# Kernel tuning notes

Measured on AMD Instinct MI355X. Metric: run time of the kernel, lower is better.

Reference implementation:

```python
import jax, jax.numpy as jnp
import numpy as np
import functools

N_NODES = 16
WIDTH = 64
C_DIM = 3
LATENT_DIM = 8
B = 131072


def build_graph(n=N_NODES, k=4, p=0.75, seed=0):
    """Watts-Strogatz-style random graph oriented low->high node id (DAG),
    mirroring build_random_graph(nodes, 1 input, 1 output, p=0.75, k=4)."""
    rng = np.random.RandomState(seed)
    edges = set()
    for i in range(n):
        for d in range(1, k // 2 + 1):
            j = (i + d) % n
            if rng.rand() < p:
                j = int(rng.randint(n))
            a, b = min(i, j), max(i, j)
            if a != b:
                edges.add((a, b))
    preds = [set() for _ in range(n)]
    for a, b in edges:
        preds[b].add(a)
    # every non-source node must have a predecessor (connectivity)
    for j in range(1, n):
        if not preds[j]:
            a = int(rng.randint(j))
            preds[j].add(a)
            edges.add((a, j))
    succs = [set() for _ in range(n)]
    for a, b in edges:
        succs[a].add(b)
    preds = [sorted(p_) for p_ in preds]
    sources = [j for j in range(n) if not preds[j]]   # receive the INR feature f
    sinks = [j for j in range(n) if not succs[j]]     # combined into the single output
    return preds, sources, sinks


def gaussian(x):
    return jnp.exp(-0.5 * x * x)

# 'large' activation set for graph nodes, assigned deterministically per node
GRAPH_ACTS = [jnp.tanh, jax.nn.elu, jax.nn.softplus, jnp.sin, gaussian]


def setup_inputs() -> dict:
    key = jax.random.key(0)
    ks = jax.random.split(key, 16)

    def nrm(k, shape, s):
        return jax.random.normal(k, shape, dtype=jnp.float32) * s

    inputs = jax.random.normal(ks[0], (B, 3, 1), dtype=jnp.float32)   # (x, y, r) coords
    latents = jax.random.normal(ks[1], (B, LATENT_DIM), dtype=jnp.float32)
    Wl = nrm(ks[2], (WIDTH, LATENT_DIM), 0.3)
    bl = jnp.zeros((WIDTH,), jnp.float32)
    Wx = nrm(ks[3], (WIDTH, 1), 1.0)
    Wy = nrm(ks[4], (WIDTH, 1), 1.0)
    Wr = nrm(ks[5], (WIDTH, 1), 1.0)
    W1 = nrm(ks[6], (WIDTH, WIDTH), 0.15)
    b1 = jnp.zeros((WIDTH,), jnp.float32)
    gW = nrm(ks[7], (N_NODES, WIDTH, WIDTH), 0.15)   # per-graph-node Linear(width,width)
    gB = jnp.zeros((N_NODES, WIDTH), jnp.float32)
    outW = nrm(ks[8], (C_DIM, WIDTH), 0.15)          # combine -> c_dim output
    outb = jnp.zeros((C_DIM,), jnp.float32)
    scale = jnp.ones((1,), jnp.float32)              # ScaleAct learnable scalar
    return {"inputs": inputs, "latents": latents, "Wl": Wl, "bl": bl, "Wx": Wx,
            "Wy": Wy, "Wr": Wr, "W1": W1, "b1": b1, "gW": gW, "gB": gB,
            "outW": outW, "outb": outb, "scale": scale}


def reference(inputs, latents, Wl, bl, Wx, Wy, Wr, W1, b1, gW, gB, outW, outb, scale):
    x, y, r = inputs[:, 0, :], inputs[:, 1, :], inputs[:, 2, :]   # each (B, 1)
    latents_ = jnp.tanh(latents @ Wl.T + bl)      # acts_start[0] = Tanh
    r_ = jax.nn.elu(r @ Wr.T)                     # acts_start[1] = ELU
    y_ = jax.nn.softplus(y @ Wy.T)                # acts_start[2] = Softplus
    x_ = jnp.tanh(x @ Wx.T)                       # acts_start[3] = Tanh
    f = gaussian(x_ + y_ + r_ + latents_)         # acts_start[4] = Gaussian
    f = jnp.sin(f @ W1.T + b1)                    # acts_start[5] = SinLayer

    # random-topology graph network: gather(sum preds) -> linear -> activation
    preds, sources, sinks = build_graph()
    hs = []
    for j in range(N_NODES):
        if j in sources:
            inp = f
        else:
            inp = functools.reduce(lambda a, b_: a + b_, [hs[i] for i in preds[j]])
        hs.append(GRAPH_ACTS[j % len(GRAPH_ACTS)](inp @ gW[j].T + gB[j]))
    agg = functools.reduce(lambda a, b_: a + b_, [hs[j] for j in sinks])
    res = (agg @ outW.T + outb) * scale           # combine + ScaleAct
    return jax.nn.sigmoid(res)                    # final_activation='sigmoid'
```

## Files before the change

kernel.cpp:

```cpp
#include <hip/hip_runtime.h>
#include <cstdint>

#define NN 16
#define W64 64
#define MT 64
#define NSTAGE 17

typedef _Float16 half8   __attribute__((ext_vector_type(8)));
typedef _Float16 half16  __attribute__((ext_vector_type(16)));
typedef float    floatx4 __attribute__((ext_vector_type(4)));

struct GraphCfg {
    unsigned pred[NN];
    unsigned sinkmask;
};

__device__ __forceinline__ float act_tanh(float x)     { return 1.0f - 2.0f / (1.0f + __expf(2.0f * x)); }
__device__ __forceinline__ float act_elu(float x)      { return x > 0.0f ? x : __expf(x) - 1.0f; }
__device__ __forceinline__ float act_softplus(float x) { return fmaxf(x, 0.0f) + __logf(1.0f + __expf(-fabsf(x))); }
__device__ __forceinline__ float act_gauss(float x)    { return __expf(-0.5f * x * x); }

__device__ __forceinline__ float apply_act(int a, float x) {
    switch (a) {
        case 0:  return act_tanh(x);
        case 1:  return act_elu(x);
        case 2:  return act_softplus(x);
        case 3:  return __sinf(x);
        default: return act_gauss(x);
    }
}

__device__ __forceinline__ half8 cvt8(float4 a, float4 b) {
    half8 h;
    h[0]=(_Float16)a.x; h[1]=(_Float16)a.y; h[2]=(_Float16)a.z; h[3]=(_Float16)a.w;
    h[4]=(_Float16)b.x; h[5]=(_Float16)b.y; h[6]=(_Float16)b.z; h[7]=(_Float16)b.w;
    return h;
}

__global__ __launch_bounds__(256, 2) void inr_mfma_kernel(
    const float* __restrict__ inputs, const float* __restrict__ latents,
    const float* __restrict__ Wl, const float* __restrict__ bl,
    const float* __restrict__ Wx, const float* __restrict__ Wy,
    const float* __restrict__ Wr, const float* __restrict__ W1,
    const float* __restrict__ b1, const float* __restrict__ gW,
    const float* __restrict__ gB, const float* __restrict__ outW,
    const float* __restrict__ outb, const float* __restrict__ scale,
    float* __restrict__ out, int Btot, GraphCfg cfg)
{
    __shared__ __align__(16) _Float16 inpbuf[2][MT * W64];
    __shared__ __align__(16) _Float16 wbuf[2][W64 * W64];

    const int tid  = threadIdx.x;
    const int lane = tid & 63;
    const int wv   = tid >> 6;
    const int q    = lane >> 4;
    const int c    = lane & 15;
    const int rowbase = wv * 16;
    const int m0   = blockIdx.x * MT;

    half16 hreg[NSTAGE];

    {
        const int em = tid >> 2, ep = tid & 3;
        int mg = m0 + em; if (mg >= Btot) mg = Btot - 1;
        const float x = inputs[mg * 3 + 0];
        const float y = inputs[mg * 3 + 1];
        const float r = inputs[mg * 3 + 2];
        const float4 l0 = *(const float4*)(latents + mg * 8);
        const float4 l1 = *(const float4*)(latents + mg * 8 + 4);
        #pragma unroll
        for (int i = 0; i < 16; ++i) {
            const int k = ep * 16 + i;
            const float4 a = *(const float4*)(Wl + k * 8);
            const float4 b = *(const float4*)(Wl + k * 8 + 4);
            float ld = bl[k];
            ld = fmaf(l0.x, a.x, ld); ld = fmaf(l0.y, a.y, ld);
            ld = fmaf(l0.z, a.z, ld); ld = fmaf(l0.w, a.w, ld);
            ld = fmaf(l1.x, b.x, ld); ld = fmaf(l1.y, b.y, ld);
            ld = fmaf(l1.z, b.z, ld); ld = fmaf(l1.w, b.w, ld);
            const float tk = act_tanh(x * Wx[k]) + act_softplus(y * Wy[k])
                           + act_elu(r * Wr[k]) + act_tanh(ld);
            inpbuf[0][em * W64 + k] = (_Float16)act_gauss(tk);
        }
    }
    {
        const float4* src = (const float4*)W1;
        const float4 f0 = src[2 * tid],       f1 = src[2 * tid + 1];
        const float4 f2 = src[2 * tid + 512], f3 = src[2 * tid + 513];
        ((half8*)wbuf[0])[tid]       = cvt8(f0, f1);
        ((half8*)wbuf[0])[tid + 256] = cvt8(f2, f3);
    }
    __syncthreads();

    #pragma unroll
    for (int s = 0; s < NSTAGE; ++s) {
        const int slot = s & 1;

        float4 nf0, nf1, nf2, nf3;
        if (s + 1 < NSTAGE) {
            const float4* src = (const float4*)(gW + s * 4096);
            nf0 = src[2 * tid];       nf1 = src[2 * tid + 1];
            nf2 = src[2 * tid + 512]; nf3 = src[2 * tid + 513];
        }

        const half8 a0 = *(const half8*)&inpbuf[slot][(rowbase + c) * W64 +  0 + q * 8];
        const half8 a1 = *(const half8*)&inpbuf[slot][(rowbase + c) * W64 + 32 + q * 8];

        floatx4 acc[4];
        #pragma unroll
        for (int t = 0; t < 4; ++t) {
            const half8 b0  = *(const half8*)&wbuf[slot][(t * 16 + c) * W64 +  0 + q * 8];
            const half8 b1f = *(const half8*)&wbuf[slot][(t * 16 + c) * W64 + 32 + q * 8];
            floatx4 z = {0.f, 0.f, 0.f, 0.f};
            z = __builtin_amdgcn_mfma_f32_16x16x32_f16(a0, b0, z, 0, 0, 0);
            z = __builtin_amdgcn_mfma_f32_16x16x32_f16(a1, b1f, z, 0, 0, 0);
            acc[t] = z;
        }

        const float* bias = (s == 0) ? b1 : (gB + (s - 1) * W64);
        const int an   = (s == 0) ? 3 : ((s - 1) % 5);
        const int hidx = (s == 0) ? 16 : (s - 1);
        #pragma unroll
        for (int t = 0; t < 4; ++t) {
            const float bs = bias[t * 16 + c];
            #pragma unroll
            for (int r = 0; r < 4; ++r) {
                const float v = apply_act(an, acc[t][r] + bs);
                hreg[hidx][t * 4 + r] = (_Float16)v;
            }
        }

        if (s + 1 < NSTAGE) {
            const int node = s;
            const unsigned pm = cfg.pred[node];
            float sf[16];
            if (pm == 0u) {
                #pragma unroll
                for (int v = 0; v < 16; ++v) sf[v] = (float)hreg[16][v];
            } else {
                #pragma unroll
                for (int v = 0; v < 16; ++v) sf[v] = 0.0f;
                #pragma unroll
                for (int i = 0; i < NN; ++i) {
                    if (pm & (1u << i)) {
                        #pragma unroll
                        for (int v = 0; v < 16; ++v) sf[v] += (float)hreg[i][v];
                    }
                }
            }
            const int wslot = (s + 1) & 1;
            #pragma unroll
            for (int t = 0; t < 4; ++t)
                #pragma unroll
                for (int r = 0; r < 4; ++r)
                    inpbuf[wslot][(rowbase + q * 4 + r) * W64 + t * 16 + c] =
                        (_Float16)sf[t * 4 + r];
            ((half8*)wbuf[wslot])[tid]       = cvt8(nf0, nf1);
            ((half8*)wbuf[wslot])[tid + 256] = cvt8(nf2, nf3);
        }
        __syncthreads();
    }

    {
        float sf[16];
        #pragma unroll
        for (int v = 0; v < 16; ++v) sf[v] = 0.0f;
        #pragma unroll
        for (int j = 0; j < NN; ++j) {
            if (cfg.sinkmask & (1u << j)) {
                #pragma unroll
                for (int v = 0; v < 16; ++v) sf[v] += (float)hreg[j][v];
            }
        }
        #pragma unroll
        for (int t = 0; t < 4; ++t)
            #pragma unroll
            for (int r = 0; r < 4; ++r)
                inpbuf[1][(rowbase + q * 4 + r) * W64 + t * 16 + c] =
                    (_Float16)sf[t * 4 + r];
    }
    __syncthreads();
    {
        const int em = tid >> 2, ep = tid & 3;
        float p0 = 0.f, p1 = 0.f, p2 = 0.f;
        #pragma unroll
        for (int h = 0; h < 2; ++h) {
            const half8 hv = *(const half8*)&inpbuf[1][em * W64 + ep * 16 + h * 8];
            #pragma unroll
            for (int i = 0; i < 8; ++i) {
                const float av = (float)hv[i];
                const int k = ep * 16 + h * 8 + i;
                p0 = fmaf(av, outW[0 * W64 + k], p0);
                p1 = fmaf(av, outW[1 * W64 + k], p1);
                p2 = fmaf(av, outW[2 * W64 + k], p2);
            }
        }
        p0 += __shfl_xor(p0, 1); p0 += __shfl_xor(p0, 2);
        p1 += __shfl_xor(p1, 1); p1 += __shfl_xor(p1, 2);
        p2 += __shfl_xor(p2, 1); p2 += __shfl_xor(p2, 2);
        const int mg = m0 + em;
        if (ep < 3 && mg < Btot) {
            const float pr = (ep == 0) ? p0 : ((ep == 1) ? p1 : p2);
            const float res = (pr + outb[ep]) * scale[0];
            out[mg * 3 + ep] = 1.0f / (1.0f + __expf(-res));
        }
    }
}

namespace {

struct NpMT {
    unsigned mt[624];
    int mti;
    explicit NpMT(unsigned s) {
        mt[0] = s;
        for (int i = 1; i < 624; ++i)
            mt[i] = 1812433253u * (mt[i-1] ^ (mt[i-1] >> 30)) + (unsigned)i;
        mti = 624;
    }
    unsigned next() {
        if (mti >= 624) {
            for (int i = 0; i < 624; ++i) {
                const unsigned y = (mt[i] & 0x80000000u) | (mt[(i+1) % 624] & 0x7fffffffu);
                unsigned v = mt[(i+397) % 624] ^ (y >> 1);
                if (y & 1u) v ^= 0x9908b0dfu;
                mt[i] = v;
            }
            mti = 0;
        }
        unsigned y = mt[mti++];
        y ^= y >> 11;
        y ^= (y << 7)  & 0x9d2c5680u;
        y ^= (y << 15) & 0xefc60000u;
        y ^= y >> 18;
        return y;
    }
    double rnd() {
        const unsigned a = next() >> 5;
        const unsigned b = next() >> 6;
        return (a * 67108864.0 + b) / 9007199254740992.0;
    }
    long randint(long n) {
        const unsigned long maxv = (unsigned long)n - 1;
        if (maxv == 0) return 0;
        unsigned long mask = maxv;
        mask |= mask >> 1;  mask |= mask >> 2;  mask |= mask >> 4;
        mask |= mask >> 8;  mask |= mask >> 16;
        unsigned long v;
        do { v = (unsigned long)next() & mask; } while (v > maxv);
        return (long)v;
    }
};

static GraphCfg build_graph_cfg() {
    NpMT rng(0u);
    bool edge[NN][NN] = {};
    for (int i = 0; i < NN; ++i) {
        for (int d = 1; d <= 2; ++d) {
            int j = (i + d) & (NN - 1);
            if (rng.rnd() < 0.75) j = (int)rng.randint(NN);
            const int a = i < j ? i : j;
            const int b = i < j ? j : i;
            if (a != b) edge[a][b] = true;
        }
    }
    GraphCfg cfg{};
    for (int a = 0; a < NN; ++a)
        for (int b = 0; b < NN; ++b)
            if (edge[a][b]) cfg.pred[b] |= 1u << a;
    for (int j = 1; j < NN; ++j) {
        if (!cfg.pred[j]) {
            const int a = (int)rng.randint(j);
            cfg.pred[j] |= 1u << a;
            edge[a][j] = true;
        }
    }
    unsigned succ[NN] = {};
    for (int a = 0; a < NN; ++a)
        for (int b = 0; b < NN; ++b)
            if (edge[a][b]) succ[a] |= 1u << b;
    cfg.sinkmask = 0u;
    for (int j = 0; j < NN; ++j)
        if (!succ[j]) cfg.sinkmask |= 1u << j;
    return cfg;
}

}

extern "C" void kernel_launch(void* const* d_in, const int* in_sizes, int n_in,
                              void* d_out, int out_size, void* d_ws, size_t ws_size,
                              hipStream_t stream)
{
    const float* inputs  = (const float*)d_in[0];
    const float* latents = (const float*)d_in[1];
    const float* Wl      = (const float*)d_in[2];
    const float* bl      = (const float*)d_in[3];
    const float* Wx      = (const float*)d_in[4];
    const float* Wy      = (const float*)d_in[5];
    const float* Wr      = (const float*)d_in[6];
    const float* W1      = (const float*)d_in[7];
    const float* b1      = (const float*)d_in[8];
    const float* gW      = (const float*)d_in[9];
    const float* gB      = (const float*)d_in[10];
    const float* outW    = (const float*)d_in[11];
    const float* outb    = (const float*)d_in[12];
    const float* scale   = (const float*)d_in[13];
    float* out = (float*)d_out;

    const int Btot = in_sizes[0] / 3;
    const GraphCfg cfg = build_graph_cfg();

    const int blocks = (Btot + MT - 1) / MT;
    inr_mfma_kernel<<<blocks, 256, 0, stream>>>(
        inputs, latents, Wl, bl, Wx, Wy, Wr, W1, b1, gW, gB, outW, outb, scale,
        out, Btot, cfg);
}
```

Before: 223.3 us.

## Pad LDS rows, sum predecessors in fp16, raise occupancy target

Pads the shared-memory activation and weight tiles from 64 to 72 halves per row so that MFMA operand loads and the strided fragment stores fall in different LDS banks. It also sums predecessor node outputs directly in packed fp16 vectors instead of converting to float and back, and raises the launch-bounds occupancy hint from 2 to 4 blocks. The fp16 accumulation loses some precision when many predecessors are summed. The higher occupancy hint may force register spills given the large per-thread hreg array.

```diff
diff --git a/kernel.cpp b/kernel.cpp
--- a/kernel.cpp
+++ b/kernel.cpp
@@ -5,6 +5,8 @@
 #define W64 64
 #define MT 64
 #define NSTAGE 17
+#define IST 72
+#define WST 72
 
 typedef _Float16 half8   __attribute__((ext_vector_type(8)));
 typedef _Float16 half16  __attribute__((ext_vector_type(16)));
@@ -37,7 +39,7 @@
     return h;
 }
 
-__global__ __launch_bounds__(256, 2) void inr_mfma_kernel(
+__global__ __launch_bounds__(256, 4) void inr_mfma_kernel(
     const float* __restrict__ inputs, const float* __restrict__ latents,
     const float* __restrict__ Wl, const float* __restrict__ bl,
     const float* __restrict__ Wx, const float* __restrict__ Wy,
@@ -47,8 +49,8 @@
     const float* __restrict__ outb, const float* __restrict__ scale,
     float* __restrict__ out, int Btot, GraphCfg cfg)
 {
-    __shared__ __align__(16) _Float16 inpbuf[2][MT * W64];
-    __shared__ __align__(16) _Float16 wbuf[2][W64 * W64];
+    __shared__ __align__(16) _Float16 inpbuf[2][MT * IST];
+    __shared__ __align__(16) _Float16 wbuf[2][W64 * WST];
 
     const int tid  = threadIdx.x;
     const int lane = tid & 63;
@@ -57,6 +59,9 @@
     const int c    = lane & 15;
     const int rowbase = wv * 16;
     const int m0   = blockIdx.x * MT;
+
+    const int srow = tid >> 3;
+    const int sc8  = tid & 7;
 
     half16 hreg[NSTAGE];
 
@@ -80,15 +85,15 @@
             ld = fmaf(l1.z, b.z, ld); ld = fmaf(l1.w, b.w, ld);
             const float tk = act_tanh(x * Wx[k]) + act_softplus(y * Wy[k])
                            + act_elu(r * Wr[k]) + act_tanh(ld);
-            inpbuf[0][em * W64 + k] = (_Float16)act_gauss(tk);
+            inpbuf[0][em * IST + k] = (_Float16)act_gauss(tk);
         }
     }
     {
         const float4* src = (const float4*)W1;
         const float4 f0 = src[2 * tid],       f1 = src[2 * tid + 1];
         const float4 f2 = src[2 * tid + 512], f3 = src[2 * tid + 513];
-        ((half8*)wbuf[0])[tid]       = cvt8(f0, f1);
-        ((half8*)wbuf[0])[tid + 256] = cvt8(f2, f3);
+        *(half8*)&wbuf[0][srow * WST + sc8 * 8]        = cvt8(f0, f1);
+        *(half8*)&wbuf[0][(srow + 32) * WST + sc8 * 8] = cvt8(f2, f3);
     }
     __syncthreads();
 
@@ -103,14 +108,14 @@
             nf2 = src[2 * tid + 512]; nf3 = src[2 * tid + 513];
         }
 
-        const half8 a0 = *(const half8*)&inpbuf[slot][(rowbase + c) * W64 +  0 + q * 8];
-        const half8 a1 = *(const half8*)&inpbuf[slot][(rowbase + c) * W64 + 32 + q * 8];
+        const half8 a0 = *(const half8*)&inpbuf[slot][(rowbase + c) * IST +  0 + q * 8];
+        const half8 a1 = *(const half8*)&inpbuf[slot][(rowbase + c) * IST + 32 + q * 8];
 
         floatx4 acc[4];
         #pragma unroll
         for (int t = 0; t < 4; ++t) {
-            const half8 b0  = *(const half8*)&wbuf[slot][(t * 16 + c) * W64 +  0 + q * 8];
-            const half8 b1f = *(const half8*)&wbuf[slot][(t * 16 + c) * W64 + 32 + q * 8];
+            const half8 b0  = *(const half8*)&wbuf[slot][(t * 16 + c) * WST +  0 + q * 8];
+            const half8 b1f = *(const half8*)&wbuf[slot][(t * 16 + c) * WST + 32 + q * 8];
             floatx4 z = {0.f, 0.f, 0.f, 0.f};
             z = __builtin_amdgcn_mfma_f32_16x16x32_f16(a0, b0, z, 0, 0, 0);
             z = __builtin_amdgcn_mfma_f32_16x16x32_f16(a1, b1f, z, 0, 0, 0);
@@ -133,18 +138,16 @@
         if (s + 1 < NSTAGE) {
             const int node = s;
             const unsigned pm = cfg.pred[node];
-            float sf[16];
+            half16 sum;
             if (pm == 0u) {
-                #pragma unroll
-                for (int v = 0; v < 16; ++v) sf[v] = (float)hreg[16][v];
+                sum = hreg[16];
             } else {
                 #pragma unroll
-                for (int v = 0; v < 16; ++v) sf[v] = 0.0f;
+                for (int v = 0; v < 16; ++v) sum[v] = (_Float16)0.0f;
                 #pragma unroll
                 for (int i = 0; i < NN; ++i) {
                     if (pm & (1u << i)) {
-                        #pragma unroll
-                        for (int v = 0; v < 16; ++v) sf[v] += (float)hreg[i][v];
+                        sum += hreg[i];
                     }
                 }
             }
@@ -153,31 +156,29 @@
             for (int t = 0; t < 4; ++t)
                 #pragma unroll
                 for (int r = 0; r < 4; ++r)
-                    inpbuf[wslot][(rowbase + q * 4 + r) * W64 + t * 16 + c] =
-                        (_Float16)sf[t * 4 + r];
-            ((half8*)wbuf[wslot])[tid]       = cvt8(nf0, nf1);
-            ((half8*)wbuf[wslot])[tid + 256] = cvt8(nf2, nf3);
+                    inpbuf[wslot][(rowbase + q * 4 + r) * IST + t * 16 + c] =
+                        sum[t * 4 + r];
+            *(half8*)&wbuf[wslot][srow * WST + sc8 * 8]        = cvt8(nf0, nf1);
+            *(half8*)&wbuf[wslot][(srow + 32) * WST + sc8 * 8] = cvt8(nf2, nf3);
         }
         __syncthreads();
     }
 
     {
-        float sf[16];
-        #pragma unroll
-        for (int v = 0; v < 16; ++v) sf[v] = 0.0f;
+        half16 sum;
+        #pragma unroll
+        for (int v = 0; v < 16; ++v) sum[v] = (_Float16)0.0f;
         #pragma unroll
         for (int j = 0; j < NN; ++j) {
             if (cfg.sinkmask & (1u << j)) {
-                #pragma unroll
-                for (int v = 0; v < 16; ++v) sf[v] += (float)hreg[j][v];
+                sum += hreg[j];
             }
         }
         #pragma unroll
         for (int t = 0; t < 4; ++t)
             #pragma unroll
             for (int r = 0; r < 4; ++r)
-                inpbuf[1][(rowbase + q * 4 + r) * W64 + t * 16 + c] =
-                    (_Float16)sf[t * 4 + r];
+                inpbuf[1][(rowbase + q * 4 + r) * IST + t * 16 + c] = sum[t * 4 + r];
     }
     __syncthreads();
     {
@@ -185,7 +186,7 @@
         float p0 = 0.f, p1 = 0.f, p2 = 0.f;
         #pragma unroll
         for (int h = 0; h < 2; ++h) {
-            const half8 hv = *(const half8*)&inpbuf[1][em * W64 + ep * 16 + h * 8];
+            const half8 hv = *(const half8*)&inpbuf[1][em * IST + ep * 16 + h * 8];
             #pragma unroll
             for (int i = 0; i < 8; ++i) {
                 const float av = (float)hv[i];
```

After: 272.7 us. +22.1%, slower.
